# Optimization experiments

Measured on AMD Instinct MI355X. Metric: run time of the kernel, lower is better.

The kernel has to match this reference:

```python
import jax, jax.numpy as jnp
import numpy as np

K = 256          # 2 ** bandwidth
NOISE = 1e-9     # init noise
T = 1.0          # temperature


def setup_inputs() -> dict:
    key = jax.random.key(0)
    k1, k2, k3 = jax.random.split(key, 3)
    inp = jax.random.normal(k1, (16, 1, 1024, 8, 8), dtype=jnp.float32)
    # per-channel resize tables (original uses fixed constants * 1.2); positive values
    resize = jax.random.uniform(k2, (3, 8, 8), dtype=jnp.float32, minval=0.05, maxval=1.5)
    t = 2.0 / K
    alpha_val = t + 3.0 * t / K
    alpha = jnp.full((8, 8), alpha_val, dtype=jnp.float32)
    beta = jnp.zeros((8, 8), dtype=jnp.float32)
    deviation = alpha / 3.0
    g = jnp.arange(-K / 2, K / 2 + 1, dtype=jnp.float32) - 0.5
    g = g.at[-1].add(1.0)
    grid_base = jnp.broadcast_to(g, (8, 8, K + 1))  # (8,8,K+1)
    # Gumbel(0,1) noise used by the training path (sampled once for determinism)
    u = jax.random.gumbel(k3, (16, 1, 1024, 8, 8, K), dtype=jnp.float32)
    return {"inp": inp, "resize": resize, "alpha": alpha, "beta": beta,
            "deviation": deviation, "grid_base": grid_base, "u": u, "i": 0}


def reference(inp, resize, alpha, beta, deviation, grid_base, u, i):
    # training-mode forward of LearnableQuantization
    x = inp / resize[i]                                    # [B,C,N,8,8]
    mean = jnp.mean(jnp.abs(x.reshape(-1, 8, 8)), axis=0)  # (8,8)
    grid = grid_base * alpha[..., None] + beta[..., None]  # (8,8,K+1)
    # sigmoid CDF over the K+1 grid points
    cdf = jax.nn.sigmoid(-(x[..., None] - grid) / deviation[..., None])  # [B,C,N,8,8,K+1]
    pi = (cdf[..., 1:] - cdf[..., :-1] + NOISE) / (cdf[..., -1:] - cdf[..., :1] + NOISE * K)
    # Gumbel-softmax over K bins (axis -1 here == axis 0 in the torch permuted layout)
    z = jnp.exp((jnp.log(pi) + u) / T)
    z = z / jnp.sum(z, axis=-1, keepdims=True)             # [B,C,N,8,8,K]
    out = jnp.sum(z * grid[:, :, :-1], axis=-1)            # [B,C,N,8,8]
    out = out * resize[i]
    nzeros = jnp.float32(0.0)
    return (out, mean, nzeros)
```

## Files before the change

kernel.cpp:

```cpp
#include <hip/hip_runtime.h>


#define KBINS 256
constexpr float NOISE = 1e-9f;

typedef float f32x4 __attribute__((ext_vector_type(4)));

__global__ __launch_bounds__(256) void lq_mean(
    const float* __restrict__ inp, const float* __restrict__ resize,
    const int* __restrict__ iptr, float* __restrict__ mean_out, int n_pos)
{
    const int c = blockIdx.x;
    const int t = threadIdx.x;
    float s = 0.0f;
    const int iters = n_pos >> 8;
    for (int k = 0; k < iters; ++k)
        s += fabsf(inp[(size_t)(t + (k << 8)) * 64 + c]);
    #pragma unroll
    for (int off = 32; off; off >>= 1) s += __shfl_xor(s, off);
    __shared__ float ws[4];
    if ((t & 63) == 0) ws[t >> 6] = s;
    __syncthreads();
    if (t == 0) {
        const float tot = ws[0] + ws[1] + ws[2] + ws[3];
        const int i0 = iptr[0];
        mean_out[c] = tot / (float)n_pos / resize[i0 * 64 + c];
        if (c == 0) mean_out[64] = 0.0f;
    }
}

__global__ __launch_bounds__(256, 4) void lq_kernel(
    const float* __restrict__ inp, const float* __restrict__ resize,
    const float* __restrict__ alpha, const float* __restrict__ beta,
    const float* __restrict__ deviation, const float* __restrict__ grid_base,
    const float* __restrict__ u, const int* __restrict__ iptr,
    float* __restrict__ out)
{
    const int lane = threadIdx.x & 63;
    const int p = blockIdx.x * (blockDim.x >> 6) + (threadIdx.x >> 6);

    const int i0 = iptr[0];
    const float rsv = resize[i0 * 64 + lane];
    const float inv_rsv = 1.0f / rsv;

    const float a    = alpha[0];
    const float bb   = beta[0];
    const float invd = 1.0f / deviation[0];

    const int k0 = lane << 2;
    const float g0 = grid_base[k0 + 0] * a + bb;
    const float g1 = grid_base[k0 + 1] * a + bb;
    const float g2 = grid_base[k0 + 2] * a + bb;
    const float g3 = grid_base[k0 + 3] * a + bb;
    const float r1 = __expf(-a * invd);
    const float rl = (lane == 63) ? r1 * r1 : r1;

    const size_t base = (size_t)p * 64;
    const float xs = inp[base + lane] * inv_rsv;

    const float* up = u + base * (size_t)KBINS + k0;

    constexpr int D = 8;
    f32x4 ub[D];
    #pragma unroll
    for (int d = 0; d < D; ++d)
        ub[d] = __builtin_nontemporal_load(
                    reinterpret_cast<const f32x4*>(up + (size_t)d * KBINS));

    float res = 0.0f;

    auto compute = [&](int c, f32x4 u4) {
        const float x = __shfl(xs, c);
        const float e0 = __expf((x - g0) * invd);
        const float e1 = e0 * r1, e2 = e1 * r1, e3 = e2 * r1, e4 = e3 * rl;
        const float c0 = __builtin_amdgcn_rcpf(1.0f + e0);
        const float c1 = __builtin_amdgcn_rcpf(1.0f + e1);
        const float c2 = __builtin_amdgcn_rcpf(1.0f + e2);
        const float c3 = __builtin_amdgcn_rcpf(1.0f + e3);
        const float c4 = __builtin_amdgcn_rcpf(1.0f + e4);

        const float z0 = (c1 - c0 + NOISE) * __expf(u4.x);
        const float z1 = (c2 - c1 + NOISE) * __expf(u4.y);
        const float z2 = (c3 - c2 + NOISE) * __expf(u4.z);
        const float z3 = (c4 - c3 + NOISE) * __expf(u4.w);

        float zn = z0 * g0 + z1 * g1 + z2 * g2 + z3 * g3;
        float zd = z0 + z1 + z2 + z3;
        #pragma unroll
        for (int off = 32; off; off >>= 1) {
            zn += __shfl_xor(zn, off);
            zd += __shfl_xor(zd, off);
        }
        const float val = zn * __builtin_amdgcn_rcpf(zd);
        res = (lane == c) ? val : res;
    };

    for (int g = 0; g < (64 / D) - 1; ++g) {
        #pragma unroll
        for (int d = 0; d < D; ++d) {
            const int c = g * D + d;
            const f32x4 un = __builtin_nontemporal_load(
                reinterpret_cast<const f32x4*>(up + (size_t)(c + D) * KBINS));
            compute(c, ub[d]);
            ub[d] = un;
        }
    }
    #pragma unroll
    for (int d = 0; d < D; ++d)
        compute(64 - D + d, ub[d]);

    out[base + lane] = res * rsv;
}

extern "C" void kernel_launch(void* const* d_in, const int* in_sizes, int n_in,
                              void* d_out, int out_size, void* d_ws, size_t ws_size,
                              hipStream_t stream) {
    const float* inp       = (const float*)d_in[0];
    const float* resize    = (const float*)d_in[1];
    const float* alpha     = (const float*)d_in[2];
    const float* beta      = (const float*)d_in[3];
    const float* deviation = (const float*)d_in[4];
    const float* grid_base = (const float*)d_in[5];
    const float* u         = (const float*)d_in[6];
    const int*   iptr      = (const int*)d_in[7];
    float* out = (float*)d_out;

    const int n_elem = in_sizes[0];
    const int n_pos  = n_elem / 64;
    float* mean_out = out + n_elem;

    hipLaunchKernelGGL(lq_mean, dim3(64), dim3(256), 0, stream,
                       inp, resize, iptr, mean_out, n_pos);

    hipLaunchKernelGGL(lq_kernel, dim3(n_pos / 4), dim3(256), 0, stream,
                       inp, resize, alpha, beta, deviation, grid_base, u, iptr,
                       out);
}
```

Before: 207.5 us.

## Fuse mean and quantize kernels; use DPP and readlane for wave reductions

The separate mean-reduction kernel is folded into the main kernel: the first 64 blocks compute the per-channel means and every other block runs the Gumbel-softmax quantization. This removes one kernel launch and the gap between the two kernels. The per-channel cross-lane reductions now use DPP quad, half-mirror and mirror steps, a ds_swizzle and one final shuffle instead of six shuffles, and the broadcast of x uses readlane instead of a shuffle. These changes cut LDS-permute traffic, but the kernel streams a very large Gumbel noise tensor and is likely limited by memory bandwidth, so the ALU-side savings may not show.

```diff
diff --git a/kernel.cpp b/kernel.cpp
--- a/kernel.cpp
+++ b/kernel.cpp
@@ -6,38 +6,49 @@
 
 typedef float f32x4 __attribute__((ext_vector_type(4)));
 
-__global__ __launch_bounds__(256) void lq_mean(
-    const float* __restrict__ inp, const float* __restrict__ resize,
-    const int* __restrict__ iptr, float* __restrict__ mean_out, int n_pos)
-{
-    const int c = blockIdx.x;
-    const int t = threadIdx.x;
-    float s = 0.0f;
-    const int iters = n_pos >> 8;
-    for (int k = 0; k < iters; ++k)
-        s += fabsf(inp[(size_t)(t + (k << 8)) * 64 + c]);
-    #pragma unroll
-    for (int off = 32; off; off >>= 1) s += __shfl_xor(s, off);
-    __shared__ float ws[4];
-    if ((t & 63) == 0) ws[t >> 6] = s;
-    __syncthreads();
-    if (t == 0) {
-        const float tot = ws[0] + ws[1] + ws[2] + ws[3];
-        const int i0 = iptr[0];
-        mean_out[c] = tot / (float)n_pos / resize[i0 * 64 + c];
-        if (c == 0) mean_out[64] = 0.0f;
-    }
+template<int CTRL>
+__device__ __forceinline__ float dpp_add(float v) {
+    const int pv = __builtin_amdgcn_update_dpp(
+        0, __float_as_int(v), CTRL, 0xF, 0xF, true);
+    return v + __int_as_float(pv);
 }
 
-__global__ __launch_bounds__(256, 4) void lq_kernel(
+__device__ __forceinline__ float swz16_add(float v) {
+    return v + __int_as_float(
+        __builtin_amdgcn_ds_swizzle(__float_as_int(v), 0x401F));
+}
+
+__global__ __launch_bounds__(256, 4) void lq_fused(
     const float* __restrict__ inp, const float* __restrict__ resize,
     const float* __restrict__ alpha, const float* __restrict__ beta,
     const float* __restrict__ deviation, const float* __restrict__ grid_base,
     const float* __restrict__ u, const int* __restrict__ iptr,
-    float* __restrict__ out)
+    float* __restrict__ out, float* __restrict__ mean_out, int n_pos)
 {
+    __shared__ float ws[4];
+
+    if (blockIdx.x < 64) {
+        const int c = blockIdx.x;
+        const int t = threadIdx.x;
+        float s = 0.0f;
+        const int iters = n_pos >> 8;
+        for (int k = 0; k < iters; ++k)
+            s += fabsf(inp[(size_t)(t + (k << 8)) * 64 + c]);
+        #pragma unroll
+        for (int off = 32; off; off >>= 1) s += __shfl_xor(s, off);
+        if ((t & 63) == 0) ws[t >> 6] = s;
+        __syncthreads();
+        if (t == 0) {
+            const float tot = ws[0] + ws[1] + ws[2] + ws[3];
+            const int i0 = iptr[0];
+            mean_out[c] = tot / (float)n_pos / resize[i0 * 64 + c];
+            if (c == 0) mean_out[64] = 0.0f;
+        }
+        return;
+    }
+
     const int lane = threadIdx.x & 63;
-    const int p = blockIdx.x * (blockDim.x >> 6) + (threadIdx.x >> 6);
+    const int p = (blockIdx.x - 64) * (blockDim.x >> 6) + (threadIdx.x >> 6);
 
     const int i0 = iptr[0];
     const float rsv = resize[i0 * 64 + lane];
@@ -70,7 +81,8 @@
     float res = 0.0f;
 
     auto compute = [&](int c, f32x4 u4) {
-        const float x = __shfl(xs, c);
+        const float x = __int_as_float(
+            __builtin_amdgcn_readlane(__float_as_int(xs), c));
         const float e0 = __expf((x - g0) * invd);
         const float e1 = e0 * r1, e2 = e1 * r1, e3 = e2 * r1, e4 = e3 * rl;
         const float c0 = __builtin_amdgcn_rcpf(1.0f + e0);
@@ -86,11 +98,13 @@
 
         float zn = z0 * g0 + z1 * g1 + z2 * g2 + z3 * g3;
         float zd = z0 + z1 + z2 + z3;
-        #pragma unroll
-        for (int off = 32; off; off >>= 1) {
-            zn += __shfl_xor(zn, off);
-            zd += __shfl_xor(zd, off);
-        }
+        zn = dpp_add<0xB1>(zn);   zd = dpp_add<0xB1>(zd);
+        zn = dpp_add<0x4E>(zn);   zd = dpp_add<0x4E>(zd);
+        zn = dpp_add<0x141>(zn);  zd = dpp_add<0x141>(zd);
+        zn = dpp_add<0x140>(zn);  zd = dpp_add<0x140>(zd);
+        zn = swz16_add(zn);       zd = swz16_add(zd);
+        zn += __shfl_xor(zn, 32); zd += __shfl_xor(zd, 32);
+
         const float val = zn * __builtin_amdgcn_rcpf(zd);
         res = (lane == c) ? val : res;
     };
@@ -129,10 +143,7 @@
     const int n_pos  = n_elem / 64;
     float* mean_out = out + n_elem;
 
-    hipLaunchKernelGGL(lq_mean, dim3(64), dim3(256), 0, stream,
-                       inp, resize, iptr, mean_out, n_pos);
-
-    hipLaunchKernelGGL(lq_kernel, dim3(n_pos / 4), dim3(256), 0, stream,
+    hipLaunchKernelGGL(lq_fused, dim3(64 + n_pos / 4), dim3(256), 0, stream,
                        inp, resize, alpha, beta, deviation, grid_base, u, iptr,
-                       out);
+                       out, mean_out, n_pos);
 }
```

Result: faster. 180.2 us (-13.2%).
